# Kernel optimization log

Measured on AMD Instinct MI355X. Metric: run time of the kernel, lower is better.

Reference implementation:

```python
import jax, jax.numpy as jnp
import numpy as np

N = 1000   # node count forced by fc1_1 in_features=1680 (see shape derivation)
E = 8000   # edges, avg degree ~8
F_IN = 6   # node feature dim (first 3 = pos, zeroed in forward)


def setup_inputs() -> dict:
    key = jax.random.key(0)
    ks = jax.random.split(key, 24)
    f = lambda k, s, sc=1.0: jax.random.normal(k, s, dtype=jnp.float32) * sc
    inp = {
        "x": f(ks[0], (N, F_IN)),
        "edge_index": jax.random.randint(ks[1], (2, E), 0, N, dtype=jnp.int64),
        # GCNConv weights (xavier-ish scale)
        "W1": f(ks[2], (F_IN, 32), 0.4), "b1": jnp.zeros((32,), jnp.float32),
        "W2": f(ks[3], (32, 32), 0.18), "b2": jnp.zeros((32,), jnp.float32),
        # Conv2d kernels, OIHW
        "k1": f(ks[4], (3, 1, 3, 2), 0.3), "kb1": jnp.zeros((3,), jnp.float32),
        "k2": f(ks[5], (6, 3, 3, 2), 0.2), "kb2": jnp.zeros((6,), jnp.float32),
        "k3": f(ks[6], (3, 6, 3, 2), 0.2), "kb3": jnp.zeros((3,), jnp.float32),
        "k4": f(ks[7], (1, 3, 3, 2), 0.2), "kb4": jnp.zeros((1,), jnp.float32),
        # FC head (torch Linear layout: [out, in])
        "fw1": f(ks[8], (1024, 1680), 0.02), "fb1": jnp.zeros((1024,), jnp.float32),
        "fw2": f(ks[9], (1024, 1024), 0.03), "fb2": jnp.zeros((1024,), jnp.float32),
        "fw3": f(ks[10], (64, 1024), 0.03), "fb3": jnp.zeros((64,), jnp.float32),
    }
    return inp


def _conv2d(x, w, b):
    out = jax.lax.conv_general_dilated(
        x, w, window_strides=(1, 1), padding="VALID",
        dimension_numbers=("NCHW", "OIHW", "NCHW"))
    return out + b[None, :, None, None]


def _maxpool2(x):  # MaxPool2d((2,1), stride=(2,1))
    return jax.lax.reduce_window(x, -jnp.inf, jax.lax.max,
                                 (1, 1, 2, 1), (1, 1, 2, 1), "VALID")


def reference(x, edge_index, W1, b1, W2, b2, k1, kb1, k2, kb2, k3, kb3, k4, kb4,
              fw1, fb1, fw2, fb2, fw3, fb3):
    num_nodes = x.shape[0]
    # forward zeroes the first 3 features (positions)
    x = x.at[:, :3].set(0.0)

    loop = jnp.arange(num_nodes)
    row = jnp.concatenate([edge_index[0], loop])
    col = jnp.concatenate([edge_index[1], loop])
    deg = jnp.zeros((num_nodes,), x.dtype).at[col].add(1.0)
    dinv = jnp.where(deg > 0, jax.lax.rsqrt(deg), 0.0)
    norm = (dinv[row] * dinv[col])[:, None]  # [E+N, 1]

    def gcn(h, W, b):
        hw = h @ W                                   # [N, 32]
        msg = hw[row] * norm                         # gather + scale
        return jax.ops.segment_sum(msg, col, num_segments=num_nodes) + b

    leaky = lambda v: jnp.where(v > 0, v, 0.2 * v)   # LeakyReLU(0.2)
    h = leaky(gcn(x, W1, b1))
    h = leaky(gcn(h, W2, b2))                        # [N, 32]

    img = h[None, None]                              # [1, 1, N, 32]
    img = _maxpool2(jax.nn.relu(_conv2d(img, k1, kb1)))   # [1,3,499,31]
    img = _maxpool2(jax.nn.relu(_conv2d(img, k2, kb2)))   # [1,6,248,30]
    img = _maxpool2(jax.nn.relu(_conv2d(img, k3, kb3)))   # [1,3,123,29]
    img = _maxpool2(jax.nn.relu(_conv2d(img, k4, kb4)))   # [1,1,60,28]

    v = img.reshape(-1)                              # [1680]
    v = v @ fw1.T + fb1                              # no activation between FCs (as in source)
    v = v @ fw2.T + fb2
    v = v @ fw3.T + fb3                              # [64]
    return v
```

## Files before the change

### kernel.cpp

```cpp
#include <hip/hip_runtime.h>

#define LEAKY(v) ((v) > 0.0f ? (v) : 0.2f * (v))

__global__ __launch_bounds__(256) void kA_prep(
        const int* __restrict__ col, float* __restrict__ deg,
        float* __restrict__ aggs ,
        float* __restrict__ outz, int n, int E) {
    int T = blockIdx.x * 256 + (int)threadIdx.x;
    int nz = 2 * n * 32;
    if (T < nz) aggs[T] = 0.0f;
    else if (T < nz + 64) outz[T - nz] = 0.0f;

    int b = blockIdx.x;
    if (b < n) {
        __shared__ int wsum[4];
        int tid = (int)threadIdx.x;
        int cnt = 0;
        for (int e = tid; e < E; e += 256) cnt += (col[e] == b) ? 1 : 0;
#pragma unroll
        for (int off = 32; off > 0; off >>= 1) cnt += __shfl_down(cnt, off, 64);
        if ((tid & 63) == 0) wsum[tid >> 6] = cnt;
        __syncthreads();
        if (tid == 0) deg[b] = (float)(wsum[0] + wsum[1] + wsum[2] + wsum[3]);
    }
}

__global__ void kB_scatter1(const float* __restrict__ x, const float* __restrict__ W1,
        const float* __restrict__ deg, const int* __restrict__ row,
        const int* __restrict__ col, float* __restrict__ agg1, int E, int n) {
    int tid = blockIdx.x * blockDim.x + threadIdx.x;
    int total = (E + n) * 32;
    if (tid >= total) return;
    int e = tid >> 5, j = tid & 31;
    int r, c; float nrm;
    if (e < E) {
        r = row[e]; c = col[e];
        nrm = (1.0f / sqrtf(deg[r] + 1.0f)) * (1.0f / sqrtf(deg[c] + 1.0f));
    } else {
        r = c = e - E;
        nrm = 1.0f / (deg[r] + 1.0f);
    }
    float val = x[r*6+3] * W1[96+j] + x[r*6+4] * W1[128+j] + x[r*6+5] * W1[160+j];
    atomicAdd(&agg1[c * 32 + j], val * nrm);
}

__global__ void kC_scatter2(const float* __restrict__ agg1, const float* __restrict__ b1,
        const float* __restrict__ W2, const float* __restrict__ deg,
        const int* __restrict__ row, const int* __restrict__ col,
        float* __restrict__ agg2, int E, int n) {
    int tid = blockIdx.x * blockDim.x + threadIdx.x;
    int total = (E + n) * 32;
    if (tid >= total) return;
    int e = tid >> 5, j = tid & 31;
    int r, c; float nrm;
    if (e < E) {
        r = row[e]; c = col[e];
        nrm = (1.0f / sqrtf(deg[r] + 1.0f)) * (1.0f / sqrtf(deg[c] + 1.0f));
    } else {
        r = c = e - E;
        nrm = 1.0f / (deg[r] + 1.0f);
    }
    const float* a = agg1 + r * 32;
    float s = 0.0f;
#pragma unroll
    for (int f = 0; f < 32; ++f) {
        float v = a[f] + b1[f];
        v = LEAKY(v);
        s += v * W2[f * 32 + j];
    }
    atomicAdd(&agg2[c * 32 + j], s * nrm);
}

__global__ __launch_bounds__(256) void kD_c3(const float* __restrict__ agg2,
        const float* __restrict__ b2,
        const float* __restrict__ k1w, const float* __restrict__ kb1,
        const float* __restrict__ k2w, const float* __restrict__ kb2,
        const float* __restrict__ k3w, const float* __restrict__ kb3,
        float* __restrict__ c3) {
    __shared__ float lc1[3][10][31];
    __shared__ float lc2[6][4][30];
    const int oh3 = blockIdx.x;
    const int tid = (int)threadIdx.x;

    for (int idx = tid; idx < 930; idx += 256) {
        int ci = idx / 310, rem = idx % 310;
        int hh = rem / 31, ow1 = rem % 31;
        int r0 = (4 * oh3 + hh) * 2;
        const float* kw = k1w + ci * 6;
        float v[4][2];
#pragma unroll
        for (int rr = 0; rr < 4; ++rr)
#pragma unroll
            for (int dc = 0; dc < 2; ++dc) {
                float u = agg2[(r0 + rr) * 32 + ow1 + dc] + b2[ow1 + dc];
                v[rr][dc] = LEAKY(u);
            }
        float a0 = v[0][0]*kw[0] + v[0][1]*kw[1] + v[1][0]*kw[2]
                 + v[1][1]*kw[3] + v[2][0]*kw[4] + v[2][1]*kw[5];
        float a1 = v[1][0]*kw[0] + v[1][1]*kw[1] + v[2][0]*kw[2]
                 + v[2][1]*kw[3] + v[3][0]*kw[4] + v[3][1]*kw[5];
        lc1[ci][hh][ow1] = fmaxf(fmaxf(a0, a1) + kb1[ci], 0.0f);
    }
    __syncthreads();

    for (int idx = tid; idx < 720; idx += 256) {
        int co2 = idx / 120, rem = idx % 120;
        int r = rem / 30, ow2 = rem % 30;
        float p0 = 0.0f, p1 = 0.0f;
#pragma unroll
        for (int ci = 0; ci < 3; ++ci) {
            const float* kw = k2w + (co2 * 3 + ci) * 6;
            const float* q0 = &lc1[ci][2*r][ow2];
            float r00 = q0[0],      r01 = q0[1];
            float r10 = q0[31],     r11 = q0[32];
            float r20 = q0[62],     r21 = q0[63];
            float r30 = q0[93],     r31 = q0[94];
            p0 += r00*kw[0] + r01*kw[1] + r10*kw[2] + r11*kw[3] + r20*kw[4] + r21*kw[5];
            p1 += r10*kw[0] + r11*kw[1] + r20*kw[2] + r21*kw[3] + r30*kw[4] + r31*kw[5];
        }
        lc2[co2][r][ow2] = fmaxf(fmaxf(p0, p1) + kb2[co2], 0.0f);
    }
    __syncthreads();

    if (tid < 87) {
        int co = tid / 29, ow3 = tid % 29;
        float A0 = 0.0f, A1 = 0.0f;
#pragma unroll
        for (int co2 = 0; co2 < 6; ++co2) {
            const float* kw3 = k3w + (co * 6 + co2) * 6;
            const float* q0 = &lc2[co2][0][ow3];
            float r00 = q0[0],      r01 = q0[1];
            float r10 = q0[30],     r11 = q0[31];
            float r20 = q0[60],     r21 = q0[61];
            float r30 = q0[90],     r31 = q0[91];
            A0 += r00*kw3[0] + r01*kw3[1] + r10*kw3[2] + r11*kw3[3] + r20*kw3[4] + r21*kw3[5];
            A1 += r10*kw3[0] + r11*kw3[1] + r20*kw3[2] + r21*kw3[3] + r30*kw3[4] + r31*kw3[5];
        }
        c3[(co * 123 + oh3) * 29 + ow3] = fmaxf(fmaxf(A0, A1) + kb3[co], 0.0f);
    }
}

__global__ __launch_bounds__(256) void kE_conv4_fc1(
        const float* __restrict__ c3, const float* __restrict__ k4,
        const float* __restrict__ kb4, const float* __restrict__ fw1,
        const float* __restrict__ fb1, float* __restrict__ f1) {
    __shared__ __align__(16) float lc4[1680];
    const int Hin = 123, Win = 29, Wo = 28;
    float kb = kb4[0];
    for (int t0 = (int)threadIdx.x; t0 < 1680; t0 += 256) {
        int ow = t0 % Wo; int oh = t0 / Wo;
        float a0 = 0.0f, a1 = 0.0f;
#pragma unroll
        for (int ci = 0; ci < 3; ++ci) {
            const float* q = c3 + (ci * Hin + 2 * oh) * Win + ow;
            const float* wp = k4 + ci * 6;
            float r00 = q[0],     r01 = q[1];
            float r10 = q[Win],   r11 = q[Win+1];
            float r20 = q[2*Win], r21 = q[2*Win+1];
            float r30 = q[3*Win], r31 = q[3*Win+1];
            a0 += r00*wp[0] + r01*wp[1] + r10*wp[2] + r11*wp[3] + r20*wp[4] + r21*wp[5];
            a1 += r10*wp[0] + r11*wp[1] + r20*wp[2] + r21*wp[3] + r30*wp[4] + r31*wp[5];
        }
        float m = fmaxf(a0, a1) + kb;
        lc4[t0] = fmaxf(m, 0.0f);
    }
    __syncthreads();
    int wv = (int)threadIdx.x >> 6, lane = (int)threadIdx.x & 63;
    int o = blockIdx.x * 4 + wv;
    const float4* wr = (const float4*)(fw1 + (size_t)o * 1680);
    const float4* vv = (const float4*)lc4;
    float s = 0.0f;
    for (int i = lane; i < 420; i += 64) {
        float4 a = vv[i], ww = wr[i];
        s += a.x*ww.x + a.y*ww.y + a.z*ww.z + a.w*ww.w;
    }
#pragma unroll
    for (int off = 32; off > 0; off >>= 1) s += __shfl_down(s, off, 64);
    if (lane == 0) f1[o] = s + fb1[o];
}

__global__ __launch_bounds__(256) void kF_fc23(const float* __restrict__ f1,
        const float* __restrict__ fw2, const float* __restrict__ fb2,
        const float* __restrict__ fw3, const float* __restrict__ fb3,
        float* __restrict__ out) {
    __shared__ float f2loc[16];
    int wv = (int)threadIdx.x >> 6, lane = (int)threadIdx.x & 63;
    int jbase = blockIdx.x * 16;
    const float4* vv = (const float4*)f1;
    for (int q = 0; q < 4; ++q) {
        int j = jbase + wv * 4 + q;
        const float4* wr = (const float4*)(fw2 + (size_t)j * 1024);
        float s = 0.0f;
#pragma unroll
        for (int i2 = 0; i2 < 4; ++i2) {
            float4 a = vv[lane + 64*i2], ww = wr[lane + 64*i2];
            s += a.x*ww.x + a.y*ww.y + a.z*ww.z + a.w*ww.w;
        }
#pragma unroll
        for (int off = 32; off > 0; off >>= 1) s += __shfl_down(s, off, 64);
        if (lane == 0) f2loc[wv * 4 + q] = s + fb2[j];
    }
    __syncthreads();
    for (int kk = 0; kk < 16; ++kk) {
        int k = wv * 16 + kk;
        float v = 0.0f;
        if (lane < 16) v = fw3[(size_t)k * 1024 + jbase + lane] * f2loc[lane];
#pragma unroll
        for (int off = 8; off > 0; off >>= 1) v += __shfl_down(v, off, 16);
        if (lane == 0) {
            if (blockIdx.x == 0) v += fb3[k];
            atomicAdd(&out[k], v);
        }
    }
}

extern "C" void kernel_launch(void* const* d_in, const int* in_sizes, int n_in,
                              void* d_out, int out_size, void* d_ws, size_t ws_size,
                              hipStream_t stream) {
    const float* x   = (const float*)d_in[0];
    const int*   ei  = (const int*)d_in[1];
    const float* W1  = (const float*)d_in[2];
    const float* b1  = (const float*)d_in[3];
    const float* W2  = (const float*)d_in[4];
    const float* b2  = (const float*)d_in[5];
    const float* k1  = (const float*)d_in[6];
    const float* kb1 = (const float*)d_in[7];
    const float* k2  = (const float*)d_in[8];
    const float* kb2 = (const float*)d_in[9];
    const float* k3  = (const float*)d_in[10];
    const float* kb3 = (const float*)d_in[11];
    const float* k4  = (const float*)d_in[12];
    const float* kb4 = (const float*)d_in[13];
    const float* fw1 = (const float*)d_in[14];
    const float* fb1 = (const float*)d_in[15];
    const float* fw2 = (const float*)d_in[16];
    const float* fb2 = (const float*)d_in[17];
    const float* fw3 = (const float*)d_in[18];
    const float* fb3 = (const float*)d_in[19];

    int n = in_sizes[0] / 6;
    int E = in_sizes[1] / 2;
    const int* row = ei;
    const int* col = ei + E;

    float* ws   = (float*)d_ws;
    float* deg  = ws;
    float* agg1 = ws + 1024;
    float* agg2 = agg1 + 32000;
    float* c3   = agg2 + 32000;
    float* f1   = c3 + 10704;

    const int B = 256;
    int st = (E + n) * 32;

    kA_prep<<<n, B, 0, stream>>>(col, deg, agg1, (float*)d_out, n, E);
    kB_scatter1<<<(st + B - 1) / B, B, 0, stream>>>(x, W1, deg, row, col, agg1, E, n);
    kC_scatter2<<<(st + B - 1) / B, B, 0, stream>>>(agg1, b1, W2, deg, row, col, agg2, E, n);
    kD_c3<<<123, B, 0, stream>>>(agg2, b2, k1, kb1, k2, kb2, k3, kb3, c3);
    kE_conv4_fc1<<<256, B, 0, stream>>>(c3, k4, kb4, fw1, fb1, f1);
    kF_fc23<<<64, B, 0, stream>>>(f1, fw2, fb2, fw3, fb3, (float*)d_out);
}
```

Measured before the change: 156.7 us.

## Fuse conv stack, conv4 and fc1 into one kernel with atomic fc1 accumulation

Merges the conv1-3 kernel and the conv4+fc1 kernel into a single launch. Each of 240 blocks computes one conv4 output row (recomputing the overlapping conv1-3 halo rows in shared memory) and adds its 28-column slice of the fc1 dot product into f1 with atomics. The fc1 bias is moved into the fc2 kernel, and f1 is zeroed in the prep kernel. This removes one launch and the c3 round trip through global memory, at the cost of redundant conv recomputation, 1024-wide atomic contention on f1, and scattered 112-byte reads of fw1 rows.

```diff
diff --git a/kernel.cpp b/kernel.cpp
--- a/kernel.cpp
+++ b/kernel.cpp
@@ -5,11 +5,11 @@
 __global__ __launch_bounds__(256) void kA_prep(
         const int* __restrict__ col, float* __restrict__ deg,
         float* __restrict__ aggs ,
-        float* __restrict__ outz, int n, int E) {
+        float* __restrict__ f1z, float* __restrict__ outz, int n, int E) {
     int T = blockIdx.x * 256 + (int)threadIdx.x;
-    int nz = 2 * n * 32;
-    if (T < nz) aggs[T] = 0.0f;
-    else if (T < nz + 64) outz[T - nz] = 0.0f;
+    if (T < 64000) aggs[T] = 0.0f;
+    else if (T < 65024) f1z[T - 64000] = 0.0f;
+    else if (T < 65088) outz[T - 65024] = 0.0f;
 
     int b = blockIdx.x;
     if (b < n) {
@@ -71,21 +71,25 @@
     atomicAdd(&agg2[c * 32 + j], s * nrm);
 }
 
-__global__ __launch_bounds__(256) void kD_c3(const float* __restrict__ agg2,
+__global__ __launch_bounds__(256) void kD_conv_fc1(const float* __restrict__ agg2,
         const float* __restrict__ b2,
         const float* __restrict__ k1w, const float* __restrict__ kb1,
         const float* __restrict__ k2w, const float* __restrict__ kb2,
         const float* __restrict__ k3w, const float* __restrict__ kb3,
-        float* __restrict__ c3) {
-    __shared__ float lc1[3][10][31];
-    __shared__ float lc2[6][4][30];
-    const int oh3 = blockIdx.x;
+        const float* __restrict__ k4w, const float* __restrict__ kb4,
+        const float* __restrict__ fw1, float* __restrict__ f1) {
+    __shared__ float lc1[3][22][31];
+    __shared__ float lc2[6][10][30];
+    __shared__ float lc3[3][4][29];
+    __shared__ __align__(16) float lc4[28];
+    const int b   = blockIdx.x >> 2;
+    const int qo  = blockIdx.x & 3;
     const int tid = (int)threadIdx.x;
 
-    for (int idx = tid; idx < 930; idx += 256) {
-        int ci = idx / 310, rem = idx % 310;
+    for (int idx = tid; idx < 2046; idx += 256) {
+        int ci = idx / 682, rem = idx % 682;
         int hh = rem / 31, ow1 = rem % 31;
-        int r0 = (4 * oh3 + hh) * 2;
+        int r0 = 16 * b + 2 * hh;
         const float* kw = k1w + ci * 6;
         float v[4][2];
 #pragma unroll
@@ -103,14 +107,14 @@
     }
     __syncthreads();
 
-    for (int idx = tid; idx < 720; idx += 256) {
-        int co2 = idx / 120, rem = idx % 120;
-        int r = rem / 30, ow2 = rem % 30;
+    for (int idx = tid; idx < 1800; idx += 256) {
+        int co2 = idx / 300, rem = idx % 300;
+        int rr = rem / 30, ow2 = rem % 30;
         float p0 = 0.0f, p1 = 0.0f;
 #pragma unroll
         for (int ci = 0; ci < 3; ++ci) {
             const float* kw = k2w + (co2 * 3 + ci) * 6;
-            const float* q0 = &lc1[ci][2*r][ow2];
+            const float* q0 = &lc1[ci][2*rr][ow2];
             float r00 = q0[0],      r01 = q0[1];
             float r10 = q0[31],     r11 = q0[32];
             float r20 = q0[62],     r21 = q0[63];
@@ -118,17 +122,18 @@
             p0 += r00*kw[0] + r01*kw[1] + r10*kw[2] + r11*kw[3] + r20*kw[4] + r21*kw[5];
             p1 += r10*kw[0] + r11*kw[1] + r20*kw[2] + r21*kw[3] + r30*kw[4] + r31*kw[5];
         }
-        lc2[co2][r][ow2] = fmaxf(fmaxf(p0, p1) + kb2[co2], 0.0f);
-    }
-    __syncthreads();
-
-    if (tid < 87) {
-        int co = tid / 29, ow3 = tid % 29;
+        lc2[co2][rr][ow2] = fmaxf(fmaxf(p0, p1) + kb2[co2], 0.0f);
+    }
+    __syncthreads();
+
+    for (int idx = tid; idx < 348; idx += 256) {
+        int co = idx / 116, rem = idx % 116;
+        int rr3 = rem / 29, ow3 = rem % 29;
         float A0 = 0.0f, A1 = 0.0f;
 #pragma unroll
         for (int co2 = 0; co2 < 6; ++co2) {
             const float* kw3 = k3w + (co * 6 + co2) * 6;
-            const float* q0 = &lc2[co2][0][ow3];
+            const float* q0 = &lc2[co2][2*rr3][ow3];
             float r00 = q0[0],      r01 = q0[1];
             float r10 = q0[30],     r11 = q0[31];
             float r20 = q0[60],     r21 = q0[61];
@@ -136,50 +141,43 @@
             A0 += r00*kw3[0] + r01*kw3[1] + r10*kw3[2] + r11*kw3[3] + r20*kw3[4] + r21*kw3[5];
             A1 += r10*kw3[0] + r11*kw3[1] + r20*kw3[2] + r21*kw3[3] + r30*kw3[4] + r31*kw3[5];
         }
-        c3[(co * 123 + oh3) * 29 + ow3] = fmaxf(fmaxf(A0, A1) + kb3[co], 0.0f);
-    }
-}
-
-__global__ __launch_bounds__(256) void kE_conv4_fc1(
-        const float* __restrict__ c3, const float* __restrict__ k4,
-        const float* __restrict__ kb4, const float* __restrict__ fw1,
-        const float* __restrict__ fb1, float* __restrict__ f1) {
-    __shared__ __align__(16) float lc4[1680];
-    const int Hin = 123, Win = 29, Wo = 28;
-    float kb = kb4[0];
-    for (int t0 = (int)threadIdx.x; t0 < 1680; t0 += 256) {
-        int ow = t0 % Wo; int oh = t0 / Wo;
+        lc3[co][rr3][ow3] = fmaxf(fmaxf(A0, A1) + kb3[co], 0.0f);
+    }
+    __syncthreads();
+
+    if (tid < 28) {
         float a0 = 0.0f, a1 = 0.0f;
 #pragma unroll
         for (int ci = 0; ci < 3; ++ci) {
-            const float* q = c3 + (ci * Hin + 2 * oh) * Win + ow;
-            const float* wp = k4 + ci * 6;
-            float r00 = q[0],     r01 = q[1];
-            float r10 = q[Win],   r11 = q[Win+1];
-            float r20 = q[2*Win], r21 = q[2*Win+1];
-            float r30 = q[3*Win], r31 = q[3*Win+1];
+            const float* wp = k4w + ci * 6;
+            const float* q = &lc3[ci][0][tid];
+            float r00 = q[0],   r01 = q[1];
+            float r10 = q[29],  r11 = q[30];
+            float r20 = q[58],  r21 = q[59];
+            float r30 = q[87],  r31 = q[88];
             a0 += r00*wp[0] + r01*wp[1] + r10*wp[2] + r11*wp[3] + r20*wp[4] + r21*wp[5];
             a1 += r10*wp[0] + r11*wp[1] + r20*wp[2] + r21*wp[3] + r30*wp[4] + r31*wp[5];
         }
-        float m = fmaxf(a0, a1) + kb;
-        lc4[t0] = fmaxf(m, 0.0f);
-    }
-    __syncthreads();
-    int wv = (int)threadIdx.x >> 6, lane = (int)threadIdx.x & 63;
-    int o = blockIdx.x * 4 + wv;
-    const float4* wr = (const float4*)(fw1 + (size_t)o * 1680);
-    const float4* vv = (const float4*)lc4;
-    float s = 0.0f;
-    for (int i = lane; i < 420; i += 64) {
-        float4 a = vv[i], ww = wr[i];
-        s += a.x*ww.x + a.y*ww.y + a.z*ww.z + a.w*ww.w;
-    }
-#pragma unroll
-    for (int off = 32; off > 0; off >>= 1) s += __shfl_down(s, off, 64);
-    if (lane == 0) f1[o] = s + fb1[o];
+        lc4[tid] = fmaxf(fmaxf(a0, a1) + kb4[0], 0.0f);
+    }
+    __syncthreads();
+
+    {
+        int o = qo * 256 + tid;
+        const float4* wr = (const float4*)(fw1 + (size_t)o * 1680 + b * 28);
+        const float4* cv = (const float4*)lc4;
+        float s = 0.0f;
+#pragma unroll
+        for (int i = 0; i < 7; ++i) {
+            float4 w4 = wr[i], c4 = cv[i];
+            s += w4.x*c4.x + w4.y*c4.y + w4.z*c4.z + w4.w*c4.w;
+        }
+        atomicAdd(&f1[o], s);
+    }
 }
 
 __global__ __launch_bounds__(256) void kF_fc23(const float* __restrict__ f1,
+        const float* __restrict__ fb1,
         const float* __restrict__ fw2, const float* __restrict__ fb2,
         const float* __restrict__ fw3, const float* __restrict__ fb3,
         float* __restrict__ out) {
@@ -187,14 +185,15 @@
     int wv = (int)threadIdx.x >> 6, lane = (int)threadIdx.x & 63;
     int jbase = blockIdx.x * 16;
     const float4* vv = (const float4*)f1;
+    const float4* bb1 = (const float4*)fb1;
     for (int q = 0; q < 4; ++q) {
         int j = jbase + wv * 4 + q;
         const float4* wr = (const float4*)(fw2 + (size_t)j * 1024);
         float s = 0.0f;
 #pragma unroll
         for (int i2 = 0; i2 < 4; ++i2) {
-            float4 a = vv[lane + 64*i2], ww = wr[lane + 64*i2];
-            s += a.x*ww.x + a.y*ww.y + a.z*ww.z + a.w*ww.w;
+            float4 a = vv[lane + 64*i2], b = bb1[lane + 64*i2], ww = wr[lane + 64*i2];
+            s += (a.x+b.x)*ww.x + (a.y+b.y)*ww.y + (a.z+b.z)*ww.z + (a.w+b.w)*ww.w;
         }
 #pragma unroll
         for (int off = 32; off > 0; off >>= 1) s += __shfl_down(s, off, 64);
@@ -247,16 +246,14 @@
     float* deg  = ws;
     float* agg1 = ws + 1024;
     float* agg2 = agg1 + 32000;
-    float* c3   = agg2 + 32000;
-    float* f1   = c3 + 10704;
+    float* f1   = agg2 + 32000;
 
     const int B = 256;
     int st = (E + n) * 32;
 
-    kA_prep<<<n, B, 0, stream>>>(col, deg, agg1, (float*)d_out, n, E);
+    kA_prep<<<n, B, 0, stream>>>(col, deg, agg1, f1, (float*)d_out, n, E);
     kB_scatter1<<<(st + B - 1) / B, B, 0, stream>>>(x, W1, deg, row, col, agg1, E, n);
     kC_scatter2<<<(st + B - 1) / B, B, 0, stream>>>(agg1, b1, W2, deg, row, col, agg2, E, n);
-    kD_c3<<<123, B, 0, stream>>>(agg2, b2, k1, kb1, k2, kb2, k3, kb3, c3);
-    kE_conv4_fc1<<<256, B, 0, stream>>>(c3, k4, kb4, fw1, fb1, f1);
-    kF_fc23<<<64, B, 0, stream>>>(f1, fw2, fb2, fw3, fb3, (float*)d_out);
-}
+    kD_conv_fc1<<<240, B, 0, stream>>>(agg2, b2, k1, kb1, k2, kb2, k3, kb3, k4, kb4, fw1, f1);
+    kF_fc23<<<64, B, 0, stream>>>(f1, fb1, fw2, fb2, fw3, fb3, (float*)d_out);
+}
```

New measurement: 155.8 us. Within noise of the previous version (-0.6%).

## Replace atomic edge-scatter GCN with per-node gather kernels

Applied to the files above, without the earlier changes.

The three prep/scatter kernels become two per-destination-node kernels. Each block scans the edge list, collects the incoming source rows in shared memory and accumulates messages in shared memory, so global atomics and the zeroing pass go away. The first kernel also builds the full degree histogram in shared memory in every block, which is redundant work of E per block. Output zeroing moves into the conv4/fc1 kernel. Each block keeps at most 128 incoming edges and silently drops any beyond that, which is a correctness risk for high in-degree nodes.

```diff
diff --git a/kernel.cpp b/kernel.cpp
--- a/kernel.cpp
+++ b/kernel.cpp
@@ -2,73 +2,100 @@
 
 #define LEAKY(v) ((v) > 0.0f ? (v) : 0.2f * (v))
 
-__global__ __launch_bounds__(256) void kA_prep(
-        const int* __restrict__ col, float* __restrict__ deg,
-        float* __restrict__ aggs ,
-        float* __restrict__ outz, int n, int E) {
-    int T = blockIdx.x * 256 + (int)threadIdx.x;
-    int nz = 2 * n * 32;
-    if (T < nz) aggs[T] = 0.0f;
-    else if (T < nz + 64) outz[T - nz] = 0.0f;
-
-    int b = blockIdx.x;
-    if (b < n) {
-        __shared__ int wsum[4];
-        int tid = (int)threadIdx.x;
-        int cnt = 0;
-        for (int e = tid; e < E; e += 256) cnt += (col[e] == b) ? 1 : 0;
-#pragma unroll
-        for (int off = 32; off > 0; off >>= 1) cnt += __shfl_down(cnt, off, 64);
-        if ((tid & 63) == 0) wsum[tid >> 6] = cnt;
-        __syncthreads();
-        if (tid == 0) deg[b] = (float)(wsum[0] + wsum[1] + wsum[2] + wsum[3]);
-    }
-}
-
-__global__ void kB_scatter1(const float* __restrict__ x, const float* __restrict__ W1,
-        const float* __restrict__ deg, const int* __restrict__ row,
-        const int* __restrict__ col, float* __restrict__ agg1, int E, int n) {
-    int tid = blockIdx.x * blockDim.x + threadIdx.x;
-    int total = (E + n) * 32;
-    if (tid >= total) return;
-    int e = tid >> 5, j = tid & 31;
-    int r, c; float nrm;
-    if (e < E) {
-        r = row[e]; c = col[e];
-        nrm = (1.0f / sqrtf(deg[r] + 1.0f)) * (1.0f / sqrtf(deg[c] + 1.0f));
-    } else {
-        r = c = e - E;
-        nrm = 1.0f / (deg[r] + 1.0f);
-    }
-    float val = x[r*6+3] * W1[96+j] + x[r*6+4] * W1[128+j] + x[r*6+5] * W1[160+j];
-    atomicAdd(&agg1[c * 32 + j], val * nrm);
-}
-
-__global__ void kC_scatter2(const float* __restrict__ agg1, const float* __restrict__ b1,
-        const float* __restrict__ W2, const float* __restrict__ deg,
+__global__ __launch_bounds__(256) void G1_gcn1(
         const int* __restrict__ row, const int* __restrict__ col,
-        float* __restrict__ agg2, int E, int n) {
-    int tid = blockIdx.x * blockDim.x + threadIdx.x;
-    int total = (E + n) * 32;
-    if (tid >= total) return;
-    int e = tid >> 5, j = tid & 31;
-    int r, c; float nrm;
-    if (e < E) {
-        r = row[e]; c = col[e];
-        nrm = (1.0f / sqrtf(deg[r] + 1.0f)) * (1.0f / sqrtf(deg[c] + 1.0f));
-    } else {
-        r = c = e - E;
-        nrm = 1.0f / (deg[r] + 1.0f);
-    }
-    const float* a = agg1 + r * 32;
-    float s = 0.0f;
-#pragma unroll
-    for (int f = 0; f < 32; ++f) {
-        float v = a[f] + b1[f];
-        v = LEAKY(v);
-        s += v * W2[f * 32 + j];
-    }
-    atomicAdd(&agg2[c * 32 + j], s * nrm);
+        const float* __restrict__ x, const float* __restrict__ W1,
+        float* __restrict__ deg, float* __restrict__ agg1, int n, int E) {
+    __shared__ int ldeg[1000];
+    __shared__ int mrow[128];
+    __shared__ int mcnt;
+    __shared__ float acc[32];
+    const int c = blockIdx.x;
+    const int tid = (int)threadIdx.x;
+
+    for (int i = tid; i < n; i += 256) ldeg[i] = 0;
+    if (tid == 0) mcnt = 0;
+    if (tid < 32) acc[tid] = 0.0f;
+    __syncthreads();
+
+    for (int e = tid; e < E; e += 256) {
+        int cc = col[e];
+        atomicAdd(&ldeg[cc], 1);
+        if (cc == c) {
+            int slot = atomicAdd(&mcnt, 1);
+            if (slot < 128) mrow[slot] = row[e];
+        }
+    }
+    __syncthreads();
+
+    const float dc = 1.0f / sqrtf((float)ldeg[c] + 1.0f);
+    const int mtot = mcnt * 32;
+    for (int idx = tid; idx < mtot; idx += 256) {
+        int m = idx >> 5, j = idx & 31;
+        int r = mrow[m];
+        float nrm = (1.0f / sqrtf((float)ldeg[r] + 1.0f)) * dc;
+        float v = x[r*6+3] * W1[96+j] + x[r*6+4] * W1[128+j] + x[r*6+5] * W1[160+j];
+        atomicAdd(&acc[j], v * nrm);
+    }
+    __syncthreads();
+
+    if (tid < 32) {
+        int j = tid;
+        float self = (x[c*6+3] * W1[96+j] + x[c*6+4] * W1[128+j] + x[c*6+5] * W1[160+j])
+                   * (1.0f / ((float)ldeg[c] + 1.0f));
+        agg1[c * 32 + j] = acc[j] + self;
+    }
+    if (tid == 32) deg[c] = (float)ldeg[c];
+}
+
+__global__ __launch_bounds__(256) void G2_gcn2(
+        const int* __restrict__ row, const int* __restrict__ col,
+        const float* __restrict__ deg, const float* __restrict__ agg1,
+        const float* __restrict__ b1, const float* __restrict__ W2,
+        float* __restrict__ agg2, int n, int E) {
+    __shared__ int mrow[128];
+    __shared__ int mcnt;
+    __shared__ float acc[32];
+    const int c = blockIdx.x;
+    const int tid = (int)threadIdx.x;
+
+    if (tid == 0) mcnt = 0;
+    if (tid < 32) acc[tid] = 0.0f;
+    __syncthreads();
+
+    for (int e = tid; e < E; e += 256) {
+        if (col[e] == c) {
+            int slot = atomicAdd(&mcnt, 1);
+            if (slot < 128) mrow[slot] = row[e];
+        }
+    }
+    __syncthreads();
+
+    const float dc = 1.0f / sqrtf(deg[c] + 1.0f);
+    const int mtot = (mcnt + 1) * 32;
+    for (int idx = tid; idx < mtot; idx += 256) {
+        int m = idx >> 5, j = idx & 31;
+        int r; float nrm;
+        if (m < mcnt) {
+            r = mrow[m];
+            nrm = (1.0f / sqrtf(deg[r] + 1.0f)) * dc;
+        } else {
+            r = c;
+            nrm = 1.0f / (deg[c] + 1.0f);
+        }
+        const float* a = agg1 + r * 32;
+        float s = 0.0f;
+#pragma unroll
+        for (int f = 0; f < 32; ++f) {
+            float v = a[f] + b1[f];
+            v = LEAKY(v);
+            s += v * W2[f * 32 + j];
+        }
+        atomicAdd(&acc[j], s * nrm);
+    }
+    __syncthreads();
+
+    if (tid < 32) agg2[c * 32 + tid] = acc[tid];
 }
 
 __global__ __launch_bounds__(256) void kD_c3(const float* __restrict__ agg2,
@@ -143,9 +170,11 @@
 __global__ __launch_bounds__(256) void kE_conv4_fc1(
         const float* __restrict__ c3, const float* __restrict__ k4,
         const float* __restrict__ kb4, const float* __restrict__ fw1,
-        const float* __restrict__ fb1, float* __restrict__ f1) {
+        const float* __restrict__ fb1, float* __restrict__ f1,
+        float* __restrict__ outz) {
     __shared__ __align__(16) float lc4[1680];
     const int Hin = 123, Win = 29, Wo = 28;
+    if (blockIdx.x == 0 && threadIdx.x < 64) outz[threadIdx.x] = 0.0f;
     float kb = kb4[0];
     for (int t0 = (int)threadIdx.x; t0 < 1680; t0 += 256) {
         int ow = t0 % Wo; int oh = t0 / Wo;
@@ -251,12 +280,10 @@
     float* f1   = c3 + 10704;
 
     const int B = 256;
-    int st = (E + n) * 32;
-
-    kA_prep<<<n, B, 0, stream>>>(col, deg, agg1, (float*)d_out, n, E);
-    kB_scatter1<<<(st + B - 1) / B, B, 0, stream>>>(x, W1, deg, row, col, agg1, E, n);
-    kC_scatter2<<<(st + B - 1) / B, B, 0, stream>>>(agg1, b1, W2, deg, row, col, agg2, E, n);
+
+    G1_gcn1<<<n, B, 0, stream>>>(row, col, x, W1, deg, agg1, n, E);
+    G2_gcn2<<<n, B, 0, stream>>>(row, col, deg, agg1, b1, W2, agg2, n, E);
     kD_c3<<<123, B, 0, stream>>>(agg2, b2, k1, kb1, k2, kb2, k3, kb3, c3);
-    kE_conv4_fc1<<<256, B, 0, stream>>>(c3, k4, kb4, fw1, fb1, f1);
+    kE_conv4_fc1<<<256, B, 0, stream>>>(c3, k4, kb4, fw1, fb1, f1, (float*)d_out);
     kF_fc23<<<64, B, 0, stream>>>(f1, fw2, fb2, fw3, fb3, (float*)d_out);
 }
```

Result: slower. 169.4 us (+8.1%).

## Precompute per-node XW before scatter and count degrees with shared-memory atomics

Applied to the files above, without the earlier changes.

Layer-2 transform (LeakyReLU plus 32x32 matmul) is now computed once per node into a buffer rather than once per edge inside the scatter, and both GCN layers reuse one generic scatter kernel. The degree count switches from one block per node scanning all edges to a single block building a shared-memory histogram with atomics. Output zeroing moves into the conv4/fc1 kernel. The trade-off is one extra kernel launch, and the degree count is now serialized in a single block.

```diff
diff --git a/kernel.cpp b/kernel.cpp
--- a/kernel.cpp
+++ b/kernel.cpp
@@ -2,32 +2,34 @@
 
 #define LEAKY(v) ((v) > 0.0f ? (v) : 0.2f * (v))
 
-__global__ __launch_bounds__(256) void kA_prep(
-        const int* __restrict__ col, float* __restrict__ deg,
-        float* __restrict__ aggs ,
-        float* __restrict__ outz, int n, int E) {
+__global__ __launch_bounds__(256) void k1_prep(const float* __restrict__ x,
+                        const int* __restrict__ col, const float* __restrict__ W1,
+                        float* __restrict__ deg,
+                        float* __restrict__ aggs ,
+                        float* __restrict__ xw, int n, int E) {
     int T = blockIdx.x * 256 + (int)threadIdx.x;
-    int nz = 2 * n * 32;
-    if (T < nz) aggs[T] = 0.0f;
-    else if (T < nz + 64) outz[T - nz] = 0.0f;
-
-    int b = blockIdx.x;
-    if (b < n) {
-        __shared__ int wsum[4];
+    int NT = gridDim.x * 256;
+    for (int i = T; i < 2 * n * 32; i += NT) aggs[i] = 0.0f;
+    for (int t = T; t < n * 32; t += NT) {
+        int j = t & 31, nn = t >> 5;
+        xw[t] = x[nn*6+3] * W1[96+j]
+              + x[nn*6+4] * W1[128+j]
+              + x[nn*6+5] * W1[160+j];
+    }
+    if (blockIdx.x == 0) {
+        __shared__ int ldeg[1024];
         int tid = (int)threadIdx.x;
-        int cnt = 0;
-        for (int e = tid; e < E; e += 256) cnt += (col[e] == b) ? 1 : 0;
-#pragma unroll
-        for (int off = 32; off > 0; off >>= 1) cnt += __shfl_down(cnt, off, 64);
-        if ((tid & 63) == 0) wsum[tid >> 6] = cnt;
+        for (int i = tid; i < 1024; i += 256) ldeg[i] = 0;
         __syncthreads();
-        if (tid == 0) deg[b] = (float)(wsum[0] + wsum[1] + wsum[2] + wsum[3]);
-    }
-}
-
-__global__ void kB_scatter1(const float* __restrict__ x, const float* __restrict__ W1,
-        const float* __restrict__ deg, const int* __restrict__ row,
-        const int* __restrict__ col, float* __restrict__ agg1, int E, int n) {
+        for (int e = tid; e < E; e += 256) atomicAdd(&ldeg[col[e]], 1);
+        __syncthreads();
+        for (int i = tid; i < n; i += 256) deg[i] = (float)ldeg[i];
+    }
+}
+
+__global__ void k_scatter(const float* __restrict__ xw, const float* __restrict__ deg,
+                          const int* __restrict__ row, const int* __restrict__ col,
+                          float* __restrict__ agg, int E, int n) {
     int tid = blockIdx.x * blockDim.x + threadIdx.x;
     int total = (E + n) * 32;
     if (tid >= total) return;
@@ -40,27 +42,15 @@
         r = c = e - E;
         nrm = 1.0f / (deg[r] + 1.0f);
     }
-    float val = x[r*6+3] * W1[96+j] + x[r*6+4] * W1[128+j] + x[r*6+5] * W1[160+j];
-    atomicAdd(&agg1[c * 32 + j], val * nrm);
-}
-
-__global__ void kC_scatter2(const float* __restrict__ agg1, const float* __restrict__ b1,
-        const float* __restrict__ W2, const float* __restrict__ deg,
-        const int* __restrict__ row, const int* __restrict__ col,
-        float* __restrict__ agg2, int E, int n) {
+    atomicAdd(&agg[c * 32 + j], xw[r * 32 + j] * nrm);
+}
+
+__global__ void k3_xw2(const float* __restrict__ agg1, const float* __restrict__ b1,
+                       const float* __restrict__ W2, float* __restrict__ xw, int n) {
     int tid = blockIdx.x * blockDim.x + threadIdx.x;
-    int total = (E + n) * 32;
-    if (tid >= total) return;
-    int e = tid >> 5, j = tid & 31;
-    int r, c; float nrm;
-    if (e < E) {
-        r = row[e]; c = col[e];
-        nrm = (1.0f / sqrtf(deg[r] + 1.0f)) * (1.0f / sqrtf(deg[c] + 1.0f));
-    } else {
-        r = c = e - E;
-        nrm = 1.0f / (deg[r] + 1.0f);
-    }
-    const float* a = agg1 + r * 32;
+    if (tid >= n * 32) return;
+    int j = tid & 31, nn = tid >> 5;
+    const float* a = agg1 + nn * 32;
     float s = 0.0f;
 #pragma unroll
     for (int f = 0; f < 32; ++f) {
@@ -68,7 +58,7 @@
         v = LEAKY(v);
         s += v * W2[f * 32 + j];
     }
-    atomicAdd(&agg2[c * 32 + j], s * nrm);
+    xw[tid] = s;
 }
 
 __global__ __launch_bounds__(256) void kD_c3(const float* __restrict__ agg2,
@@ -140,12 +130,14 @@
     }
 }
 
-__global__ __launch_bounds__(256) void kE_conv4_fc1(
+__global__ __launch_bounds__(256) void k8_conv4_fc1(
         const float* __restrict__ c3, const float* __restrict__ k4,
         const float* __restrict__ kb4, const float* __restrict__ fw1,
-        const float* __restrict__ fb1, float* __restrict__ f1) {
+        const float* __restrict__ fb1, float* __restrict__ f1,
+        float* __restrict__ outz) {
     __shared__ __align__(16) float lc4[1680];
     const int Hin = 123, Win = 29, Wo = 28;
+    if (blockIdx.x == 0 && threadIdx.x < 64) outz[threadIdx.x] = 0.0f;
     float kb = kb4[0];
     for (int t0 = (int)threadIdx.x; t0 < 1680; t0 += 256) {
         int ow = t0 % Wo; int oh = t0 / Wo;
@@ -247,16 +239,18 @@
     float* deg  = ws;
     float* agg1 = ws + 1024;
     float* agg2 = agg1 + 32000;
-    float* c3   = agg2 + 32000;
+    float* xw   = agg2 + 32000;
+    float* c3   = xw + 32000;
     float* f1   = c3 + 10704;
 
     const int B = 256;
     int st = (E + n) * 32;
 
-    kA_prep<<<n, B, 0, stream>>>(col, deg, agg1, (float*)d_out, n, E);
-    kB_scatter1<<<(st + B - 1) / B, B, 0, stream>>>(x, W1, deg, row, col, agg1, E, n);
-    kC_scatter2<<<(st + B - 1) / B, B, 0, stream>>>(agg1, b1, W2, deg, row, col, agg2, E, n);
+    k1_prep<<<256, B, 0, stream>>>(x, col, W1, deg, agg1, xw, n, E);
+    k_scatter<<<(st + B - 1) / B, B, 0, stream>>>(xw, deg, row, col, agg1, E, n);
+    k3_xw2<<<(n * 32 + B - 1) / B, B, 0, stream>>>(agg1, b1, W2, xw, n);
+    k_scatter<<<(st + B - 1) / B, B, 0, stream>>>(xw, deg, row, col, agg2, E, n);
     kD_c3<<<123, B, 0, stream>>>(agg2, b2, k1, kb1, k2, kb2, k3, kb3, c3);
-    kE_conv4_fc1<<<256, B, 0, stream>>>(c3, k4, kb4, fw1, fb1, f1);
+    k8_conv4_fc1<<<256, B, 0, stream>>>(c3, k4, kb4, fw1, fb1, f1, (float*)d_out);
     kF_fc23<<<64, B, 0, stream>>>(f1, fw2, fb2, fw3, fb3, (float*)d_out);
 }
```

After: 164.4 us. +4.9%, slower.
